# Performance work log

Hardware: AMD Instinct MI355X
Metric: run time of the kernel (lower is better)

## Reference

```python
import jax, jax.numpy as jnp
import numpy as np


def expm2(M):
    """Closed-form exponential of a batch of 2x2 matrices M[..., 2, 2].

    exp(M) = e^m * (f*I + g*(M - m*I)) with m = tr(M)/2,
    delta = m^2 - det(M), and (f, g) = (cosh s, sinh s / s) if delta >= 0
    else (cos s, sin s / s) with s = sqrt(|delta|). Identical math to
    torch.matrix_exp for 2x2 inputs.
    """
    a, b, c, d = M[..., 0, 0], M[..., 0, 1], M[..., 1, 0], M[..., 1, 1]
    m = 0.5 * (a + d)
    delta = m * m - (a * d - b * c)
    s = jnp.sqrt(jnp.abs(delta))
    s_safe = jnp.maximum(s, 1e-12)
    pos = delta >= 0
    f = jnp.where(pos, jnp.cosh(s), jnp.cos(s))
    g = jnp.where(pos, jnp.sinh(s_safe), jnp.sin(s_safe)) / s_safe
    em = jnp.exp(m)
    I = jnp.eye(2, dtype=M.dtype)
    N = M - m[..., None, None] * I
    return em[..., None, None] * (f[..., None, None] * I + g[..., None, None] * N)


def setup_inputs() -> dict:
    key = jax.random.key(0)
    k_x0, = jax.random.split(key, 1)
    T, B = 8192, 4096
    t = jnp.arange(T, dtype=jnp.float32) * 0.01  # monotone time grid
    x0 = jax.random.normal(k_x0, (2, B), dtype=jnp.float32)
    return {
        "t": t,
        "x0": x0,
        "omega_sq": jnp.float32(1.2),
        "gamma_0": jnp.float32(0.35),
        "gamma_amp": jnp.float32(0.15),
        "omega_d": jnp.float32(1.1),
    }


def reference(t, x0, omega_sq, gamma_0, gamma_amp, omega_d):
    # Magnus-0 midpoint rule: x_i = exp(dt_i * A(t_mid_i)) @ x_{i-1}
    dt = t[1:] - t[:-1]                      # [T-1]
    tm = t[:-1] + 0.5 * dt                   # midpoint times
    gamma = gamma_0 * (1.0 + gamma_amp * jnp.sin(omega_d * tm))
    zeros = jnp.zeros_like(dt)
    # M_i = dt_i * A(tm_i) = [[0, dt], [-omega_sq*dt, -gamma*dt]]
    M = jnp.stack(
        [jnp.stack([zeros, dt], axis=-1),
         jnp.stack([-omega_sq * dt, -gamma * dt], axis=-1)],
        axis=-2,
    )  # [T-1, 2, 2]
    E = expm2(M)                             # [T-1, 2, 2] step propagators

    def step(x, Ei):
        xn = Ei @ x                          # [2, B]
        return xn, xn

    _, traj = jax.lax.scan(step, x0, E)      # [T-1, 2, B]
    return jnp.concatenate([x0[None], traj], axis=0)  # [T, 2, B]
```

## Files before the change

### kernel.cpp

```cpp
#include <hip/hip_runtime.h>
#include <math.h>


#define CS  64
#define TPB 256

__global__ void compute_E(const float* __restrict__ t,
                          const float* __restrict__ p_w2,
                          const float* __restrict__ p_g0,
                          const float* __restrict__ p_gamp,
                          const float* __restrict__ p_od,
                          float4* __restrict__ E, int nsteps) {
    int j = blockIdx.x * blockDim.x + threadIdx.x;
    if (j >= nsteps) return;
    double w2 = (double)p_w2[0], g0 = (double)p_g0[0];
    double gamp = (double)p_gamp[0], od = (double)p_od[0];
    double t0 = (double)t[j], t1 = (double)t[j + 1];
    double dt = t1 - t0;
    double tm = t0 + 0.5 * dt;
    double gamma = g0 * (1.0 + gamp * sin(od * tm));
    double m = -0.5 * gamma * dt;
    double delta = m * m - w2 * dt * dt;
    double s = sqrt(fabs(delta));
    double ss = fmax(s, 1e-12);
    double f, g;
    if (delta >= 0.0) { f = cosh(s); g = sinh(ss) / ss; }
    else              { f = cos(s);  g = sin(ss) / ss;  }
    double em = exp(m);
    float4 e;
    e.x = (float)(em * (f - g * m));
    e.y = (float)(em * (g * dt));
    e.z = (float)(em * (-g * w2 * dt));
    e.w = (float)(em * (f + g * m));
    E[j] = e;
}

__global__ void chunk_scan(const float4* __restrict__ E,
                           float4* __restrict__ Q,
                           int nsteps, int nch) {
    __shared__ double Ms[TPB][4];
    int c = threadIdx.x;
    if (c < nch) {
        double m00 = 1, m01 = 0, m10 = 0, m11 = 1;
        int j0 = c * CS;
        int j1 = min(j0 + CS, nsteps);
        for (int j = j0; j < j1; ++j) {
            float4 e = E[j];
            double e00 = e.x, e01 = e.y, e10 = e.z, e11 = e.w;
            double n00 = e00 * m00 + e01 * m10;
            double n01 = e00 * m01 + e01 * m11;
            double n10 = e10 * m00 + e11 * m10;
            double n11 = e10 * m01 + e11 * m11;
            m00 = n00; m01 = n01; m10 = n10; m11 = n11;
        }
        Ms[c][0] = m00; Ms[c][1] = m01; Ms[c][2] = m10; Ms[c][3] = m11;
    }
    __syncthreads();
    if (threadIdx.x == 0) {
        double q00 = 1, q01 = 0, q10 = 0, q11 = 1;
        for (int cc = 0; cc < nch; ++cc) {
            Q[cc] = make_float4((float)q00, (float)q01, (float)q10, (float)q11);
            double a00 = Ms[cc][0], a01 = Ms[cc][1], a10 = Ms[cc][2], a11 = Ms[cc][3];
            double n00 = a00 * q00 + a01 * q10;
            double n01 = a00 * q01 + a01 * q11;
            double n10 = a10 * q00 + a11 * q10;
            double n11 = a10 * q01 + a11 * q11;
            q00 = n00; q01 = n01; q10 = n10; q11 = n11;
        }
    }
}

__global__ __launch_bounds__(TPB) void propagate(
        const float4* __restrict__ E,
        const float4* __restrict__ Q,
        const float* __restrict__ x0,
        float* __restrict__ out,
        int nsteps, int B, int bgroups) {
    __shared__ float4 Es[CS];
    int c  = blockIdx.x / bgroups;
    int bg = blockIdx.x % bgroups;
    int b  = bg * TPB + threadIdx.x;
    int j0 = c * CS;
    int n  = min(CS, nsteps - j0);
    if (threadIdx.x < n) Es[threadIdx.x] = E[j0 + threadIdx.x];
    __syncthreads();
    if (b >= B) return;

    float4 q = Q[c];
    float xa0 = x0[b], xb0 = x0[B + b];
    float xa = q.x * xa0 + q.y * xb0;
    float xb = q.z * xa0 + q.w * xb0;

    if (c == 0) {
        out[b] = xa0;
        out[B + b] = xb0;
    }

    float* o = out + (size_t)(j0 + 1) * 2 * (size_t)B + b;
    #pragma unroll 4
    for (int jj = 0; jj < n; ++jj) {
        float4 e = Es[jj];
        float na = e.x * xa + e.y * xb;
        float nb = e.z * xa + e.w * xb;
        xa = na; xb = nb;
        o[0] = xa;
        o[B] = xb;
        o += 2 * B;
    }
}

extern "C" void kernel_launch(void* const* d_in, const int* in_sizes, int n_in,
                              void* d_out, int out_size, void* d_ws, size_t ws_size,
                              hipStream_t stream) {
    const float* t    = (const float*)d_in[0];
    const float* x0   = (const float*)d_in[1];
    const float* w2   = (const float*)d_in[2];
    const float* g0   = (const float*)d_in[3];
    const float* gamp = (const float*)d_in[4];
    const float* od   = (const float*)d_in[5];
    float* out = (float*)d_out;

    const int T = in_sizes[0];
    const int B = in_sizes[1] / 2;
    const int nsteps = T - 1;
    const int nch = (nsteps + CS - 1) / CS;
    const int bgroups = (B + TPB - 1) / TPB;

    float4* E = (float4*)d_ws;
    float4* Q = (float4*)((char*)d_ws + ((size_t)nsteps * 16 + 255 & ~(size_t)255));

    compute_E<<<(nsteps + TPB - 1) / TPB, TPB, 0, stream>>>(t, w2, g0, gamp, od, E, nsteps);
    chunk_scan<<<1, TPB, 0, stream>>>(E, Q, nsteps, nch);
    propagate<<<nch * bgroups, TPB, 0, stream>>>(E, Q, x0, out, nsteps, B, bgroups);
}
```

Measured before the change: 279.1 us.

## Fuse step propagator and chunk products via wave shuffles, vectorize propagate stores

The compute_E and serial chunk_scan kernels are merged into one chunk_E kernel. It computes each step matrix and reduces every 64-step chunk's product with a wave-level shuffle tree in double precision. The single-thread serial per-chunk loop and one kernel launch go away. Each propagate block now computes its own prefix by serially multiplying the preceding chunk products from shared memory, which adds redundant work to later chunks. Each thread also handles two batch columns with float2 loads and nontemporal stores, halving the block count.

```diff
diff --git a/kernel.cpp b/kernel.cpp
--- a/kernel.cpp
+++ b/kernel.cpp
@@ -2,109 +2,137 @@
 #include <math.h>
 
 
-#define CS  64
-#define TPB 256
+#define CS    64
+#define TPB   256
+#define MAXCH 256
 
-__global__ void compute_E(const float* __restrict__ t,
-                          const float* __restrict__ p_w2,
-                          const float* __restrict__ p_g0,
-                          const float* __restrict__ p_gamp,
-                          const float* __restrict__ p_od,
-                          float4* __restrict__ E, int nsteps) {
-    int j = blockIdx.x * blockDim.x + threadIdx.x;
-    if (j >= nsteps) return;
-    double w2 = (double)p_w2[0], g0 = (double)p_g0[0];
-    double gamp = (double)p_gamp[0], od = (double)p_od[0];
-    double t0 = (double)t[j], t1 = (double)t[j + 1];
-    double dt = t1 - t0;
-    double tm = t0 + 0.5 * dt;
-    double gamma = g0 * (1.0 + gamp * sin(od * tm));
-    double m = -0.5 * gamma * dt;
-    double delta = m * m - w2 * dt * dt;
-    double s = sqrt(fabs(delta));
-    double ss = fmax(s, 1e-12);
-    double f, g;
-    if (delta >= 0.0) { f = cosh(s); g = sinh(ss) / ss; }
-    else              { f = cos(s);  g = sin(ss) / ss;  }
-    double em = exp(m);
-    float4 e;
-    e.x = (float)(em * (f - g * m));
-    e.y = (float)(em * (g * dt));
-    e.z = (float)(em * (-g * w2 * dt));
-    e.w = (float)(em * (f + g * m));
-    E[j] = e;
+typedef float fvec2 __attribute__((ext_vector_type(2)));
+
+__global__ __launch_bounds__(64) void chunk_E(
+        const float* __restrict__ t,
+        const float* __restrict__ p_w2,
+        const float* __restrict__ p_g0,
+        const float* __restrict__ p_gamp,
+        const float* __restrict__ p_od,
+        float4* __restrict__ E,
+        double* __restrict__ M,
+        int nsteps) {
+    const int c = blockIdx.x;
+    const int j = c * CS + threadIdx.x;
+    double e00 = 1.0, e01 = 0.0, e10 = 0.0, e11 = 1.0;
+    if (j < nsteps) {
+        double w2 = (double)p_w2[0], g0 = (double)p_g0[0];
+        double gamp = (double)p_gamp[0], od = (double)p_od[0];
+        double t0 = (double)t[j], t1 = (double)t[j + 1];
+        double dt = t1 - t0;
+        double tm = t0 + 0.5 * dt;
+        double gamma = g0 * (1.0 + gamp * sin(od * tm));
+        double m = -0.5 * gamma * dt;
+        double delta = m * m - w2 * dt * dt;
+        double s = sqrt(fabs(delta));
+        double ss = fmax(s, 1e-12);
+        double f, g;
+        if (delta >= 0.0) {
+            f = cosh(s); g = sinh(ss) / ss;
+        } else {
+            double sn, cz;
+            sincos(ss, &sn, &cz);
+            f = cz; g = sn / ss;
+        }
+        double em = exp(m);
+        e00 = em * (f - g * m);
+        e01 = em * (g * dt);
+        e10 = em * (-g * w2 * dt);
+        e11 = em * (f + g * m);
+        E[j] = make_float4((float)e00, (float)e01, (float)e10, (float)e11);
+    }
+    #pragma unroll
+    for (int k = 0; k < 6; ++k) {
+        const int hi = (threadIdx.x >> k) & 1;
+        double p00 = __shfl_xor(e00, 1 << k, 64);
+        double p01 = __shfl_xor(e01, 1 << k, 64);
+        double p10 = __shfl_xor(e10, 1 << k, 64);
+        double p11 = __shfl_xor(e11, 1 << k, 64);
+        double a00 = hi ? e00 : p00, a01 = hi ? e01 : p01;
+        double a10 = hi ? e10 : p10, a11 = hi ? e11 : p11;
+        double b00 = hi ? p00 : e00, b01 = hi ? p01 : e01;
+        double b10 = hi ? p10 : e10, b11 = hi ? p11 : e11;
+        e00 = a00 * b00 + a01 * b10;
+        e01 = a00 * b01 + a01 * b11;
+        e10 = a10 * b00 + a11 * b10;
+        e11 = a10 * b01 + a11 * b11;
+    }
+    if (threadIdx.x == 0) {
+        M[4 * c + 0] = e00; M[4 * c + 1] = e01;
+        M[4 * c + 2] = e10; M[4 * c + 3] = e11;
+    }
 }
 
-__global__ void chunk_scan(const float4* __restrict__ E,
-                           float4* __restrict__ Q,
-                           int nsteps, int nch) {
-    __shared__ double Ms[TPB][4];
-    int c = threadIdx.x;
-    if (c < nch) {
-        double m00 = 1, m01 = 0, m10 = 0, m11 = 1;
-        int j0 = c * CS;
-        int j1 = min(j0 + CS, nsteps);
-        for (int j = j0; j < j1; ++j) {
-            float4 e = E[j];
-            double e00 = e.x, e01 = e.y, e10 = e.z, e11 = e.w;
-            double n00 = e00 * m00 + e01 * m10;
-            double n01 = e00 * m01 + e01 * m11;
-            double n10 = e10 * m00 + e11 * m10;
-            double n11 = e10 * m01 + e11 * m11;
-            m00 = n00; m01 = n01; m10 = n10; m11 = n11;
-        }
-        Ms[c][0] = m00; Ms[c][1] = m01; Ms[c][2] = m10; Ms[c][3] = m11;
-    }
+__global__ __launch_bounds__(TPB) void propagate(
+        const float4* __restrict__ E,
+        const double* __restrict__ M,
+        const float* __restrict__ x0,
+        float* __restrict__ out,
+        int nsteps, int B, int bgroups) {
+    __shared__ float4 Es[CS];
+    __shared__ double Ml[MAXCH][4];
+    __shared__ double qsh[4];
+    const int c   = blockIdx.x / bgroups;
+    const int bg  = blockIdx.x % bgroups;
+    const int tid = threadIdx.x;
+    const int j0  = c * CS;
+    const int n   = min(CS, nsteps - j0);
+
+    if (tid < n) Es[tid] = E[j0 + tid];
+    for (int i = tid; i < 4 * c; i += TPB)
+        Ml[i >> 2][i & 3] = M[i];
     __syncthreads();
-    if (threadIdx.x == 0) {
+
+    if (tid == 0) {
         double q00 = 1, q01 = 0, q10 = 0, q11 = 1;
-        for (int cc = 0; cc < nch; ++cc) {
-            Q[cc] = make_float4((float)q00, (float)q01, (float)q10, (float)q11);
-            double a00 = Ms[cc][0], a01 = Ms[cc][1], a10 = Ms[cc][2], a11 = Ms[cc][3];
+        for (int cc = 0; cc < c; ++cc) {
+            double a00 = Ml[cc][0], a01 = Ml[cc][1];
+            double a10 = Ml[cc][2], a11 = Ml[cc][3];
             double n00 = a00 * q00 + a01 * q10;
             double n01 = a00 * q01 + a01 * q11;
             double n10 = a10 * q00 + a11 * q10;
             double n11 = a10 * q01 + a11 * q11;
             q00 = n00; q01 = n01; q10 = n10; q11 = n11;
         }
+        qsh[0] = q00; qsh[1] = q01; qsh[2] = q10; qsh[3] = q11;
     }
-}
+    __syncthreads();
+    const float q00 = (float)qsh[0], q01 = (float)qsh[1];
+    const float q10 = (float)qsh[2], q11 = (float)qsh[3];
 
-__global__ __launch_bounds__(TPB) void propagate(
-        const float4* __restrict__ E,
-        const float4* __restrict__ Q,
-        const float* __restrict__ x0,
-        float* __restrict__ out,
-        int nsteps, int B, int bgroups) {
-    __shared__ float4 Es[CS];
-    int c  = blockIdx.x / bgroups;
-    int bg = blockIdx.x % bgroups;
-    int b  = bg * TPB + threadIdx.x;
-    int j0 = c * CS;
-    int n  = min(CS, nsteps - j0);
-    if (threadIdx.x < n) Es[threadIdx.x] = E[j0 + threadIdx.x];
-    __syncthreads();
+    const int b = 2 * (bg * TPB + tid);
     if (b >= B) return;
 
-    float4 q = Q[c];
-    float xa0 = x0[b], xb0 = x0[B + b];
-    float xa = q.x * xa0 + q.y * xb0;
-    float xb = q.z * xa0 + q.w * xb0;
+    const float2 xr0 = *(const float2*)(x0 + b);
+    const float2 xr1 = *(const float2*)(x0 + B + b);
+    float a0 = q00 * xr0.x + q01 * xr1.x;
+    float c0 = q10 * xr0.x + q11 * xr1.x;
+    float a1 = q00 * xr0.y + q01 * xr1.y;
+    float c1 = q10 * xr0.y + q11 * xr1.y;
 
     if (c == 0) {
-        out[b] = xa0;
-        out[B + b] = xb0;
+        *(float2*)(out + b) = xr0;
+        *(float2*)(out + B + b) = xr1;
     }
 
     float* o = out + (size_t)(j0 + 1) * 2 * (size_t)B + b;
     #pragma unroll 4
     for (int jj = 0; jj < n; ++jj) {
         float4 e = Es[jj];
-        float na = e.x * xa + e.y * xb;
-        float nb = e.z * xa + e.w * xb;
-        xa = na; xb = nb;
-        o[0] = xa;
-        o[B] = xb;
+        float na0 = e.x * a0 + e.y * c0;
+        float nc0 = e.z * a0 + e.w * c0;
+        float na1 = e.x * a1 + e.y * c1;
+        float nc1 = e.z * a1 + e.w * c1;
+        a0 = na0; c0 = nc0; a1 = na1; c1 = nc1;
+        fvec2 r0; r0.x = a0; r0.y = a1;
+        fvec2 r1; r1.x = c0; r1.y = c1;
+        __builtin_nontemporal_store(r0, (fvec2*)o);
+        __builtin_nontemporal_store(r1, (fvec2*)(o + B));
         o += 2 * B;
     }
 }
@@ -124,12 +152,11 @@
     const int B = in_sizes[1] / 2;
     const int nsteps = T - 1;
     const int nch = (nsteps + CS - 1) / CS;
-    const int bgroups = (B + TPB - 1) / TPB;
+    const int bgroups = (B + 2 * TPB - 1) / (2 * TPB);
 
     float4* E = (float4*)d_ws;
-    float4* Q = (float4*)((char*)d_ws + ((size_t)nsteps * 16 + 255 & ~(size_t)255));
+    double* M = (double*)((char*)d_ws + (((size_t)nsteps * 16 + 255) & ~(size_t)255));
 
-    compute_E<<<(nsteps + TPB - 1) / TPB, TPB, 0, stream>>>(t, w2, g0, gamp, od, E, nsteps);
-    chunk_scan<<<1, TPB, 0, stream>>>(E, Q, nsteps, nch);
-    propagate<<<nch * bgroups, TPB, 0, stream>>>(E, Q, x0, out, nsteps, B, bgroups);
+    chunk_E<<<nch, 64, 0, stream>>>(t, w2, g0, gamp, od, E, M, nsteps);
+    propagate<<<nch * bgroups, TPB, 0, stream>>>(E, M, x0, out, nsteps, B, bgroups);
 }
```

Result: no change. 274.6 us (-1.6%).
